# Performance work log

Measured on AMD Instinct MI355X. Metric: run time of the kernel, lower is better.

Reference implementation:

```python
import jax, jax.numpy as jnp
import numpy as np

D_MODEL = 512
NUM_HEADS = 8
VOCAB = 32000
B, TQ, TS = 4, 512, 512


def setup_inputs() -> dict:
    key = jax.random.key(0)
    ks = jax.random.split(key, 12)
    s = 1.0 / np.sqrt(D_MODEL)
    inp = {
        "src_vocab_size": VOCAB,
        "dec_output": jax.random.normal(ks[0], (B, TQ, D_MODEL), jnp.float32),
        "enc_output": jax.random.normal(ks[1], (B, TS, D_MODEL), jnp.float32),
        "src": jax.random.randint(ks[2], (B, TS), 0, VOCAB),
        "p1": jax.random.uniform(ks[3], (B, TQ, VOCAB), jnp.float32),
        # fcQ: d_model -> d_model (xavier)
        "WfcQ": jax.random.normal(ks[4], (D_MODEL, D_MODEL), jnp.float32) * s,
        "bfcQ": jnp.zeros((D_MODEL,), jnp.float32),
        # MHA query / key projections (V and output proj skipped in copy mode)
        "Wq": jax.random.normal(ks[5], (D_MODEL, D_MODEL), jnp.float32) * s,
        "bq": jnp.zeros((D_MODEL,), jnp.float32),
        "Wk": jax.random.normal(ks[6], (D_MODEL, D_MODEL), jnp.float32) * s,
        "bk": jnp.zeros((D_MODEL,), jnp.float32),
        # fcw: d_model -> 1 gate
        "Wfcw": jax.random.normal(ks[7], (1, D_MODEL), jnp.float32) * s,
        "bfcw": jnp.zeros((1,), jnp.float32),
    }
    return inp


def reference(src_vocab_size, dec_output, enc_output, src, p1,
              WfcQ, bfcQ, Wq, bq, Wk, bk, Wfcw, bfcw):
    b, tq, d = dec_output.shape
    h = NUM_HEADS
    dh = d // h
    # copy_query = fcQ(dec_output)
    cq = dec_output @ WfcQ.T + bfcQ
    # per-head Q, K projections
    Q = (cq @ Wq.T + bq).reshape(b, tq, h, dh).transpose(0, 2, 1, 3)          # [b,h,tq,dh]
    K = (enc_output @ Wk.T + bk).reshape(b, -1, h, dh).transpose(0, 2, 1, 3)  # [b,h,ts,dh]
    scale = 1.0 / jnp.sqrt(jnp.asarray(dh, dec_output.dtype))
    scores = jnp.einsum('bhqd,bhkd->bhqk', Q, K) * scale
    attn = jax.nn.softmax(scores, axis=-1).mean(axis=1)  # [b,tq,ts] head-averaged
    # attn @ one_hot(src, vocab)  ==  scatter-add of attn weights by src token id
    def scatter_copy(a, s):  # a: [tq,ts], s: [ts]
        return jax.ops.segment_sum(a.T, s, num_segments=src_vocab_size).T  # [tq,vocab]
    a_output = jax.vmap(scatter_copy)(attn, src)  # [b,tq,vocab]
    p2 = jax.nn.softmax(a_output, axis=-1)
    w = jax.nn.sigmoid(dec_output @ Wfcw.T + bfcw)  # [b,tq,1]
    return p2 * w + (1.0 - w) * p1
```

## Files before the change

kernel.cpp:

```cpp
#include <hip/hip_runtime.h>

constexpr int BATCH = 4;
constexpr int SEQ   = 512;
constexpr int DM    = 512;
constexpr int NH    = 8;
constexpr int HD    = 64;
constexpr int NV    = 32000;
constexpr int NROWS = BATCH * SEQ;

__device__ __forceinline__ float wave_reduce_max(float v) {
#pragma unroll
  for (int o = 32; o > 0; o >>= 1) v = fmaxf(v, __shfl_down(v, o, 64));
  return v;
}
__device__ __forceinline__ float wave_reduce_sum(float v) {
#pragma unroll
  for (int o = 32; o > 0; o >>= 1) v += __shfl_down(v, o, 64);
  return v;
}

__global__ __launch_bounds__(256)
void gemm_bias_kernel(const float* __restrict__ A, const float* __restrict__ W,
                      const float* __restrict__ bias, float* __restrict__ C,
                      int M, int N, int K) {
  __shared__ float As[16][68];
  __shared__ float Ws[16][68];
  const int tid = threadIdx.x;
  const int tx = tid & 15, ty = tid >> 4;
  const int m0 = blockIdx.y << 6, n0 = blockIdx.x << 6;
  const int r = tid >> 2;
  const int c = (tid & 3) << 2;
  float acc[4][4] = {};
  for (int k0 = 0; k0 < K; k0 += 16) {
    float4 av = *(const float4*)(A + (size_t)(m0 + r) * K + k0 + c);
    float4 wv = *(const float4*)(W + (size_t)(n0 + r) * K + k0 + c);
    As[c + 0][r] = av.x; As[c + 1][r] = av.y; As[c + 2][r] = av.z; As[c + 3][r] = av.w;
    Ws[c + 0][r] = wv.x; Ws[c + 1][r] = wv.y; Ws[c + 2][r] = wv.z; Ws[c + 3][r] = wv.w;
    __syncthreads();
#pragma unroll
    for (int kk = 0; kk < 16; ++kk) {
      float4 a4 = *(const float4*)(&As[kk][ty << 2]);
      float4 b4 = *(const float4*)(&Ws[kk][tx << 2]);
      float a[4] = {a4.x, a4.y, a4.z, a4.w};
      float b[4] = {b4.x, b4.y, b4.z, b4.w};
#pragma unroll
      for (int i = 0; i < 4; ++i)
#pragma unroll
        for (int j = 0; j < 4; ++j) acc[i][j] = fmaf(a[i], b[j], acc[i][j]);
    }
    __syncthreads();
  }
#pragma unroll
  for (int i = 0; i < 4; ++i) {
    const int m = m0 + (ty << 2) + i;
#pragma unroll
    for (int j = 0; j < 4; ++j) {
      const int n = n0 + (tx << 2) + j;
      C[(size_t)m * N + n] = acc[i][j] + bias[n];
    }
  }
}

__global__ __launch_bounds__(256)
void scores_kernel(const float* __restrict__ Qlin, const float* __restrict__ Klin,
                   float* __restrict__ scores) {
  const int bh = blockIdx.z, bb = bh >> 3, h = bh & 7;
  const int tq0 = blockIdx.y << 6, ts0 = blockIdx.x << 6;
  __shared__ float Qs[64 * 65];
  __shared__ float Ks[64 * 65];
  const int tid = threadIdx.x;
#pragma unroll
  for (int i = 0; i < 4; ++i) {
    const int idx = tid + (i << 8);
    const int rr = idx >> 4, cc = (idx & 15) << 2;
    float4 qv = *(const float4*)(Qlin + (size_t)(bb * SEQ + tq0 + rr) * DM + h * HD + cc);
    Qs[rr * 65 + cc + 0] = qv.x; Qs[rr * 65 + cc + 1] = qv.y;
    Qs[rr * 65 + cc + 2] = qv.z; Qs[rr * 65 + cc + 3] = qv.w;
    float4 kv = *(const float4*)(Klin + (size_t)(bb * SEQ + ts0 + rr) * DM + h * HD + cc);
    Ks[rr * 65 + cc + 0] = kv.x; Ks[rr * 65 + cc + 1] = kv.y;
    Ks[rr * 65 + cc + 2] = kv.z; Ks[rr * 65 + cc + 3] = kv.w;
  }
  __syncthreads();
  const int tx = tid & 15, ty = tid >> 4;
  float acc[4][4] = {};
#pragma unroll 4
  for (int k = 0; k < 64; ++k) {
    float a[4], b[4];
#pragma unroll
    for (int i = 0; i < 4; ++i) a[i] = Qs[(ty * 4 + i) * 65 + k];
#pragma unroll
    for (int j = 0; j < 4; ++j) b[j] = Ks[(tx * 4 + j) * 65 + k];
#pragma unroll
    for (int i = 0; i < 4; ++i)
#pragma unroll
      for (int j = 0; j < 4; ++j) acc[i][j] = fmaf(a[i], b[j], acc[i][j]);
  }
#pragma unroll
  for (int i = 0; i < 4; ++i) {
    const int tq = tq0 + ty * 4 + i;
#pragma unroll
    for (int j = 0; j < 4; ++j) {
      const int ts = ts0 + tx * 4 + j;
      scores[((size_t)bh * SEQ + tq) * SEQ + ts] = acc[i][j] * 0.125f;
    }
  }
}

__global__ __launch_bounds__(256)
void softmax_mean_kernel(const float* __restrict__ scores, float* __restrict__ attn) {
  __shared__ float redm[4], reds[4];
  const int row = blockIdx.x;
  const int bb = row >> 9, tq = row & 511;
  const int tid = threadIdx.x;
  const int wid = tid >> 6, lane = tid & 63;
  float acc0 = 0.f, acc1 = 0.f;
  for (int h = 0; h < NH; ++h) {
    const float* srow = scores + ((size_t)(bb * NH + h) * SEQ + tq) * SEQ;
    const float s0 = srow[tid], s1 = srow[tid + 256];
    float m = wave_reduce_max(fmaxf(s0, s1));
    __syncthreads();
    if (lane == 0) redm[wid] = m;
    __syncthreads();
    m = fmaxf(fmaxf(redm[0], redm[1]), fmaxf(redm[2], redm[3]));
    const float e0 = __expf(s0 - m), e1 = __expf(s1 - m);
    float s = wave_reduce_sum(e0 + e1);
    __syncthreads();
    if (lane == 0) reds[wid] = s;
    __syncthreads();
    s = reds[0] + reds[1] + reds[2] + reds[3];
    const float inv = 1.f / s;
    acc0 = fmaf(e0, inv, acc0);
    acc1 = fmaf(e1, inv, acc1);
  }
  attn[(size_t)row * SEQ + tid]       = acc0 * 0.125f;
  attn[(size_t)row * SEQ + tid + 256] = acc1 * 0.125f;
}

__global__ void build_map_kernel(const int* __restrict__ src, int* __restrict__ map) {
  const int bb = blockIdx.x, ts = threadIdx.x;
  const int v = src[bb * SEQ + ts];
  atomicCAS(&map[(size_t)bb * NV + v], -1, ts);
}

__global__ void scatter_kernel(const float* __restrict__ attn, const int* __restrict__ src,
                               const int* __restrict__ map, float* __restrict__ aslots) {
  const int row = blockIdx.x, bb = row >> 9, ts = threadIdx.x;
  const int v = src[bb * SEQ + ts];
  const int rep = map[(size_t)bb * NV + v];
  atomicAdd(&aslots[(size_t)row * SEQ + rep], attn[(size_t)row * SEQ + ts]);
}

__global__ __launch_bounds__(256)
void row_stats_kernel(float* __restrict__ aslots, const float* __restrict__ dec,
                      const float* __restrict__ Wfcw, const float* __restrict__ bfcw,
                      float* __restrict__ row_a, float* __restrict__ row_b) {
  __shared__ float red1[4], red2[4];
  const int row = blockIdx.x, tid = threadIdx.x;
  const int wid = tid >> 6, lane = tid & 63;
  const float a0 = aslots[(size_t)row * SEQ + tid];
  const float a1 = aslots[(size_t)row * SEQ + tid + 256];
  const float e0 = __expf(a0), e1 = __expf(a1);
  aslots[(size_t)row * SEQ + tid] = e0;
  aslots[(size_t)row * SEQ + tid + 256] = e1;
  const float es = wave_reduce_sum(e0 + e1);
  const float d = dec[(size_t)row * DM + tid] * Wfcw[tid] +
                  dec[(size_t)row * DM + tid + 256] * Wfcw[tid + 256];
  const float ds = wave_reduce_sum(d);
  if (lane == 0) { red1[wid] = es; red2[wid] = ds; }
  __syncthreads();
  if (tid == 0) {
    const float esum = red1[0] + red1[1] + red1[2] + red1[3];
    const float dsum = red2[0] + red2[1] + red2[2] + red2[3] + bfcw[0];
    const float w = 1.f / (1.f + __expf(-dsum));
    const float denom = (float)(NV - SEQ) + esum;
    row_a[row] = 1.f - w;
    row_b[row] = w / denom;
  }
}

__global__ __launch_bounds__(256)
void final_kernel(const float* __restrict__ p1, const int* __restrict__ map,
                  const float* __restrict__ expa, const float* __restrict__ row_a,
                  const float* __restrict__ row_b, float* __restrict__ out) {
  const size_t g = (size_t)blockIdx.x * 256 + threadIdx.x;
  const int row = (int)(g / (NV / 4));
  const int q4  = (int)(g % (NV / 4));
  const int bb = row >> 9;
  const float4 p = ((const float4*)p1)[g];
  const int4 m = *(const int4*)(map + (size_t)bb * NV + (q4 << 2));
  const float ra = row_a[row], rb = row_b[row];
  const float* ea = expa + (size_t)row * SEQ;
  const float e0 = (m.x >= 0) ? ea[m.x] : 1.f;
  const float e1 = (m.y >= 0) ? ea[m.y] : 1.f;
  const float e2 = (m.z >= 0) ? ea[m.z] : 1.f;
  const float e3 = (m.w >= 0) ? ea[m.w] : 1.f;
  float4 o;
  o.x = fmaf(ra, p.x, rb * e0);
  o.y = fmaf(ra, p.y, rb * e1);
  o.z = fmaf(ra, p.z, rb * e2);
  o.w = fmaf(ra, p.w, rb * e3);
  ((float4*)out)[g] = o;
}

extern "C" void kernel_launch(void* const* d_in, const int* in_sizes, int n_in,
                              void* d_out, int out_size, void* d_ws, size_t ws_size,
                              hipStream_t stream) {
  const float* dec  = (const float*)d_in[1];
  const float* enc  = (const float*)d_in[2];
  const int*   src  = (const int*)d_in[3];
  const float* p1   = (const float*)d_in[4];
  const float* WfcQ = (const float*)d_in[5];
  const float* bfcQ = (const float*)d_in[6];
  const float* Wq   = (const float*)d_in[7];
  const float* bq   = (const float*)d_in[8];
  const float* Wk   = (const float*)d_in[9];
  const float* bk   = (const float*)d_in[10];
  const float* Wfcw = (const float*)d_in[11];
  const float* bfcw = (const float*)d_in[12];
  float* out = (float*)d_out;

  char* ws = (char*)d_ws;
  float* qlin   = (float*)(ws);
  float* klin   = (float*)(ws + (size_t)(4  << 20));
  float* attn   = (float*)(ws + (size_t)(8  << 20));
  float* aslots = (float*)(ws + (size_t)(12 << 20));
  int*   map    = (int*)  (ws + (size_t)(16 << 20));
  float* row_a  = (float*)(ws + (size_t)(17 << 20));
  float* row_b  = (float*)(ws + (size_t)(17 << 20) + 16384);
  float* scores = (float*)(ws + (size_t)(18 << 20));
  float* cq     = scores;

  hipMemsetAsync(map, 0xFF, (size_t)BATCH * NV * sizeof(int), stream);
  hipMemsetAsync(aslots, 0, (size_t)NROWS * SEQ * sizeof(float), stream);

  build_map_kernel<<<BATCH, SEQ, 0, stream>>>(src, map);

  dim3 gg(DM / 64, NROWS / 64);
  gemm_bias_kernel<<<gg, 256, 0, stream>>>(dec, WfcQ, bfcQ, cq,   NROWS, DM, DM);
  gemm_bias_kernel<<<gg, 256, 0, stream>>>(cq,  Wq,   bq,   qlin, NROWS, DM, DM);
  gemm_bias_kernel<<<gg, 256, 0, stream>>>(enc, Wk,   bk,   klin, NROWS, DM, DM);

  dim3 sg(SEQ / 64, SEQ / 64, BATCH * NH);
  scores_kernel<<<sg, 256, 0, stream>>>(qlin, klin, scores);

  softmax_mean_kernel<<<NROWS, 256, 0, stream>>>(scores, attn);
  scatter_kernel<<<NROWS, SEQ, 0, stream>>>(attn, src, map, aslots);
  row_stats_kernel<<<NROWS, 256, 0, stream>>>(aslots, dec, Wfcw, bfcw, row_a, row_b);

  final_kernel<<<(NROWS * (NV / 4)) / 256, 256, 0, stream>>>(p1, map, aslots, row_a, row_b, out);
}
```

Measured before the change: 588.2 us.

## Use bf16 MFMA GEMMs, fold fcQ into Wq, fuse softmax-scatter-stats

Inputs and K weights are converted to bf16, and the two Q-side linear layers are folded into one weight matrix and bias, so Q and K are computed by a single bf16 MFMA GEMM launch. The score computation also uses MFMA and writes bf16 scores. Head-softmax, head averaging, scatter into slots, exponentiation and the gate statistics are fused into one block-per-row kernel that uses shared-memory atomics. This removes fp32 FMA GEMMs, several intermediate buffers and launches, and the aslots memset, at the cost of bf16 rounding in the projections and scores.

```diff
diff --git a/kernel.cpp b/kernel.cpp
--- a/kernel.cpp
+++ b/kernel.cpp
@@ -4,10 +4,12 @@
 constexpr int SEQ   = 512;
 constexpr int DM    = 512;
 constexpr int NH    = 8;
-constexpr int HD    = 64;
 constexpr int NV    = 32000;
 constexpr int NROWS = BATCH * SEQ;
 
+typedef short short8 __attribute__((ext_vector_type(8)));
+typedef float floatx4 __attribute__((ext_vector_type(4)));
+
 __device__ __forceinline__ float wave_reduce_max(float v) {
 #pragma unroll
   for (int o = 32; o > 0; o >>= 1) v = fmaxf(v, __shfl_down(v, o, 64));
@@ -18,122 +20,162 @@
   for (int o = 32; o > 0; o >>= 1) v += __shfl_down(v, o, 64);
   return v;
 }
-
-__global__ __launch_bounds__(256)
-void gemm_bias_kernel(const float* __restrict__ A, const float* __restrict__ W,
-                      const float* __restrict__ bias, float* __restrict__ C,
-                      int M, int N, int K) {
+__device__ __forceinline__ unsigned short f2bf(float f) {
+  unsigned u = __float_as_uint(f);
+  u += 0x7FFFu + ((u >> 16) & 1u);
+  return (unsigned short)(u >> 16);
+}
+__device__ __forceinline__ float bf2f(unsigned short b) {
+  return __uint_as_float(((unsigned)b) << 16);
+}
+
+__global__ __launch_bounds__(256)
+void convert_bf16_kernel(const float* __restrict__ in, unsigned short* __restrict__ out, int n4) {
+  const int i = blockIdx.x * 256 + threadIdx.x;
+  if (i < n4) {
+    const float4 v = ((const float4*)in)[i];
+    ushort4 o;
+    o.x = f2bf(v.x); o.y = f2bf(v.y); o.z = f2bf(v.z); o.w = f2bf(v.w);
+    ((ushort4*)out)[i] = o;
+  }
+}
+
+__global__ __launch_bounds__(256)
+void wfold_kernel(const float* __restrict__ Wq, const float* __restrict__ WfcQ,
+                  unsigned short* __restrict__ Wqc) {
   __shared__ float As[16][68];
-  __shared__ float Ws[16][68];
+  __shared__ float Bs[16][68];
+  const int tid = threadIdx.x, tx = tid & 15, ty = tid >> 4;
+  const int m0 = blockIdx.y << 6, n0 = blockIdx.x << 6;
+  const int r = tid >> 2, c = (tid & 3) << 2;
+  float acc[4][4] = {};
+  for (int k0 = 0; k0 < DM; k0 += 16) {
+    const float4 av = *(const float4*)(Wq + (size_t)(m0 + r) * DM + k0 + c);
+    As[c + 0][r] = av.x; As[c + 1][r] = av.y; As[c + 2][r] = av.z; As[c + 3][r] = av.w;
+    const float4 bv = *(const float4*)(WfcQ + (size_t)(k0 + ty) * DM + n0 + (tx << 2));
+    *(float4*)(&Bs[ty][tx << 2]) = bv;
+    __syncthreads();
+#pragma unroll
+    for (int kk = 0; kk < 16; ++kk) {
+      const float4 a4 = *(const float4*)(&As[kk][ty << 2]);
+      const float4 b4 = *(const float4*)(&Bs[kk][tx << 2]);
+      const float a[4] = {a4.x, a4.y, a4.z, a4.w};
+      const float b[4] = {b4.x, b4.y, b4.z, b4.w};
+#pragma unroll
+      for (int i = 0; i < 4; ++i)
+#pragma unroll
+        for (int j = 0; j < 4; ++j) acc[i][j] = fmaf(a[i], b[j], acc[i][j]);
+    }
+    __syncthreads();
+  }
+#pragma unroll
+  for (int i = 0; i < 4; ++i)
+#pragma unroll
+    for (int j = 0; j < 4; ++j)
+      Wqc[(size_t)(m0 + (ty << 2) + i) * DM + n0 + (tx << 2) + j] = f2bf(acc[i][j]);
+}
+
+__global__ __launch_bounds__(512)
+void bias_fold_kernel(const float* __restrict__ Wq, const float* __restrict__ bfcQ,
+                      const float* __restrict__ bq, float* __restrict__ bq2) {
+  const int tid = threadIdx.x, h = tid >> 6, l = tid & 63;
+  const int n = blockIdx.x * 8 + h;
+  float s = 0.f;
+#pragma unroll
+  for (int t = 0; t < 8; ++t) {
+    const int j = l + 64 * t;
+    s = fmaf(Wq[(size_t)n * DM + j], bfcQ[j], s);
+  }
+  s = wave_reduce_sum(s);
+  if (l == 0) bq2[n] = bq[n] + s;
+}
+
+__global__ __launch_bounds__(256)
+void gemm_mfma_kernel(const unsigned short* __restrict__ A0, const unsigned short* __restrict__ W0,
+                      const float* __restrict__ b0, unsigned short* __restrict__ C0,
+                      const unsigned short* __restrict__ A1, const unsigned short* __restrict__ W1,
+                      const float* __restrict__ b1, unsigned short* __restrict__ C1) {
+  const unsigned short* A; const unsigned short* W; const float* bias; unsigned short* C;
+  if (blockIdx.z == 0) { A = A0; W = W0; bias = b0; C = C0; }
+  else                 { A = A1; W = W1; bias = b1; C = C1; }
+  const int m0 = blockIdx.y << 6, n0 = blockIdx.x << 6;
+  __shared__ __align__(16) unsigned short As[64 * 72];
+  __shared__ __align__(16) unsigned short Ws[64 * 72];
   const int tid = threadIdx.x;
-  const int tx = tid & 15, ty = tid >> 4;
-  const int m0 = blockIdx.y << 6, n0 = blockIdx.x << 6;
-  const int r = tid >> 2;
-  const int c = (tid & 3) << 2;
-  float acc[4][4] = {};
-  for (int k0 = 0; k0 < K; k0 += 16) {
-    float4 av = *(const float4*)(A + (size_t)(m0 + r) * K + k0 + c);
-    float4 wv = *(const float4*)(W + (size_t)(n0 + r) * K + k0 + c);
-    As[c + 0][r] = av.x; As[c + 1][r] = av.y; As[c + 2][r] = av.z; As[c + 3][r] = av.w;
-    Ws[c + 0][r] = wv.x; Ws[c + 1][r] = wv.y; Ws[c + 2][r] = wv.z; Ws[c + 3][r] = wv.w;
+  const int wv = tid >> 6, l = tid & 63;
+  const int lm = l & 15, lq = l >> 4;
+  floatx4 acc[4] = {};
+  for (int k0 = 0; k0 < DM; k0 += 64) {
+#pragma unroll
+    for (int i = 0; i < 2; ++i) {
+      const int ch = tid + (i << 8);
+      const int row = ch >> 3, c8 = (ch & 7) << 3;
+      *(int4*)(&As[row * 72 + c8]) = *(const int4*)(A + (size_t)(m0 + row) * DM + k0 + c8);
+      *(int4*)(&Ws[row * 72 + c8]) = *(const int4*)(W + (size_t)(n0 + row) * DM + k0 + c8);
+    }
     __syncthreads();
 #pragma unroll
-    for (int kk = 0; kk < 16; ++kk) {
-      float4 a4 = *(const float4*)(&As[kk][ty << 2]);
-      float4 b4 = *(const float4*)(&Ws[kk][tx << 2]);
-      float a[4] = {a4.x, a4.y, a4.z, a4.w};
-      float b[4] = {b4.x, b4.y, b4.z, b4.w};
-#pragma unroll
-      for (int i = 0; i < 4; ++i)
-#pragma unroll
-        for (int j = 0; j < 4; ++j) acc[i][j] = fmaf(a[i], b[j], acc[i][j]);
+    for (int ks = 0; ks < 64; ks += 32) {
+      const short8 a = *(const short8*)(&As[(16 * wv + lm) * 72 + ks + lq * 8]);
+#pragma unroll
+      for (int c = 0; c < 4; ++c) {
+        const short8 b = *(const short8*)(&Ws[(16 * c + lm) * 72 + ks + lq * 8]);
+        acc[c] = __builtin_amdgcn_mfma_f32_16x16x32_bf16(a, b, acc[c], 0, 0, 0);
+      }
     }
     __syncthreads();
   }
 #pragma unroll
-  for (int i = 0; i < 4; ++i) {
-    const int m = m0 + (ty << 2) + i;
-#pragma unroll
-    for (int j = 0; j < 4; ++j) {
-      const int n = n0 + (tx << 2) + j;
-      C[(size_t)m * N + n] = acc[i][j] + bias[n];
-    }
-  }
-}
-
-__global__ __launch_bounds__(256)
-void scores_kernel(const float* __restrict__ Qlin, const float* __restrict__ Klin,
-                   float* __restrict__ scores) {
+  for (int c = 0; c < 4; ++c) {
+    const int col = n0 + 16 * c + lm;
+    const float bv = bias[col];
+#pragma unroll
+    for (int r = 0; r < 4; ++r) {
+      const int row = m0 + 16 * wv + lq * 4 + r;
+      C[(size_t)row * DM + col] = f2bf(acc[c][r] + bv);
+    }
+  }
+}
+
+__global__ __launch_bounds__(256)
+void scores_mfma_kernel(const unsigned short* __restrict__ Q, const unsigned short* __restrict__ Kk,
+                        unsigned short* __restrict__ scores) {
   const int bh = blockIdx.z, bb = bh >> 3, h = bh & 7;
   const int tq0 = blockIdx.y << 6, ts0 = blockIdx.x << 6;
-  __shared__ float Qs[64 * 65];
-  __shared__ float Ks[64 * 65];
+  __shared__ __align__(16) unsigned short Qs[64 * 72];
+  __shared__ __align__(16) unsigned short Ks[64 * 72];
   const int tid = threadIdx.x;
-#pragma unroll
-  for (int i = 0; i < 4; ++i) {
-    const int idx = tid + (i << 8);
-    const int rr = idx >> 4, cc = (idx & 15) << 2;
-    float4 qv = *(const float4*)(Qlin + (size_t)(bb * SEQ + tq0 + rr) * DM + h * HD + cc);
-    Qs[rr * 65 + cc + 0] = qv.x; Qs[rr * 65 + cc + 1] = qv.y;
-    Qs[rr * 65 + cc + 2] = qv.z; Qs[rr * 65 + cc + 3] = qv.w;
-    float4 kv = *(const float4*)(Klin + (size_t)(bb * SEQ + ts0 + rr) * DM + h * HD + cc);
-    Ks[rr * 65 + cc + 0] = kv.x; Ks[rr * 65 + cc + 1] = kv.y;
-    Ks[rr * 65 + cc + 2] = kv.z; Ks[rr * 65 + cc + 3] = kv.w;
+  const int wv = tid >> 6, l = tid & 63;
+  const int lm = l & 15, lq = l >> 4;
+#pragma unroll
+  for (int i = 0; i < 2; ++i) {
+    const int ch = tid + (i << 8);
+    const int row = ch >> 3, c8 = (ch & 7) << 3;
+    *(int4*)(&Qs[row * 72 + c8]) =
+        *(const int4*)(Q + (size_t)(bb * SEQ + tq0 + row) * DM + h * 64 + c8);
+    *(int4*)(&Ks[row * 72 + c8]) =
+        *(const int4*)(Kk + (size_t)(bb * SEQ + ts0 + row) * DM + h * 64 + c8);
   }
   __syncthreads();
-  const int tx = tid & 15, ty = tid >> 4;
-  float acc[4][4] = {};
-#pragma unroll 4
-  for (int k = 0; k < 64; ++k) {
-    float a[4], b[4];
-#pragma unroll
-    for (int i = 0; i < 4; ++i) a[i] = Qs[(ty * 4 + i) * 65 + k];
-#pragma unroll
-    for (int j = 0; j < 4; ++j) b[j] = Ks[(tx * 4 + j) * 65 + k];
-#pragma unroll
-    for (int i = 0; i < 4; ++i)
-#pragma unroll
-      for (int j = 0; j < 4; ++j) acc[i][j] = fmaf(a[i], b[j], acc[i][j]);
-  }
-#pragma unroll
-  for (int i = 0; i < 4; ++i) {
-    const int tq = tq0 + ty * 4 + i;
-#pragma unroll
-    for (int j = 0; j < 4; ++j) {
-      const int ts = ts0 + tx * 4 + j;
-      scores[((size_t)bh * SEQ + tq) * SEQ + ts] = acc[i][j] * 0.125f;
-    }
-  }
-}
-
-__global__ __launch_bounds__(256)
-void softmax_mean_kernel(const float* __restrict__ scores, float* __restrict__ attn) {
-  __shared__ float redm[4], reds[4];
-  const int row = blockIdx.x;
-  const int bb = row >> 9, tq = row & 511;
-  const int tid = threadIdx.x;
-  const int wid = tid >> 6, lane = tid & 63;
-  float acc0 = 0.f, acc1 = 0.f;
-  for (int h = 0; h < NH; ++h) {
-    const float* srow = scores + ((size_t)(bb * NH + h) * SEQ + tq) * SEQ;
-    const float s0 = srow[tid], s1 = srow[tid + 256];
-    float m = wave_reduce_max(fmaxf(s0, s1));
-    __syncthreads();
-    if (lane == 0) redm[wid] = m;
-    __syncthreads();
-    m = fmaxf(fmaxf(redm[0], redm[1]), fmaxf(redm[2], redm[3]));
-    const float e0 = __expf(s0 - m), e1 = __expf(s1 - m);
-    float s = wave_reduce_sum(e0 + e1);
-    __syncthreads();
-    if (lane == 0) reds[wid] = s;
-    __syncthreads();
-    s = reds[0] + reds[1] + reds[2] + reds[3];
-    const float inv = 1.f / s;
-    acc0 = fmaf(e0, inv, acc0);
-    acc1 = fmaf(e1, inv, acc1);
-  }
-  attn[(size_t)row * SEQ + tid]       = acc0 * 0.125f;
-  attn[(size_t)row * SEQ + tid + 256] = acc1 * 0.125f;
+  floatx4 acc[4] = {};
+#pragma unroll
+  for (int ks = 0; ks < 64; ks += 32) {
+    const short8 a = *(const short8*)(&Qs[(16 * wv + lm) * 72 + ks + lq * 8]);
+#pragma unroll
+    for (int c = 0; c < 4; ++c) {
+      const short8 b = *(const short8*)(&Ks[(16 * c + lm) * 72 + ks + lq * 8]);
+      acc[c] = __builtin_amdgcn_mfma_f32_16x16x32_bf16(a, b, acc[c], 0, 0, 0);
+    }
+  }
+#pragma unroll
+  for (int c = 0; c < 4; ++c) {
+    const int ts = ts0 + 16 * c + lm;
+#pragma unroll
+    for (int r = 0; r < 4; ++r) {
+      const int tq = tq0 + 16 * wv + lq * 4 + r;
+      scores[((size_t)bh * SEQ + tq) * SEQ + ts] = f2bf(acc[c][r] * 0.125f);
+    }
+  }
 }
 
 __global__ void build_map_kernel(const int* __restrict__ src, int* __restrict__ map) {
@@ -142,39 +184,63 @@
   atomicCAS(&map[(size_t)bb * NV + v], -1, ts);
 }
 
-__global__ void scatter_kernel(const float* __restrict__ attn, const int* __restrict__ src,
-                               const int* __restrict__ map, float* __restrict__ aslots) {
-  const int row = blockIdx.x, bb = row >> 9, ts = threadIdx.x;
-  const int v = src[bb * SEQ + ts];
-  const int rep = map[(size_t)bb * NV + v];
-  atomicAdd(&aslots[(size_t)row * SEQ + rep], attn[(size_t)row * SEQ + ts]);
-}
-
-__global__ __launch_bounds__(256)
-void row_stats_kernel(float* __restrict__ aslots, const float* __restrict__ dec,
-                      const float* __restrict__ Wfcw, const float* __restrict__ bfcw,
-                      float* __restrict__ row_a, float* __restrict__ row_b) {
-  __shared__ float red1[4], red2[4];
-  const int row = blockIdx.x, tid = threadIdx.x;
-  const int wid = tid >> 6, lane = tid & 63;
-  const float a0 = aslots[(size_t)row * SEQ + tid];
-  const float a1 = aslots[(size_t)row * SEQ + tid + 256];
-  const float e0 = __expf(a0), e1 = __expf(a1);
-  aslots[(size_t)row * SEQ + tid] = e0;
-  aslots[(size_t)row * SEQ + tid + 256] = e1;
-  const float es = wave_reduce_sum(e0 + e1);
-  const float d = dec[(size_t)row * DM + tid] * Wfcw[tid] +
-                  dec[(size_t)row * DM + tid + 256] * Wfcw[tid + 256];
-  const float ds = wave_reduce_sum(d);
-  if (lane == 0) { red1[wid] = es; red2[wid] = ds; }
+__global__ __launch_bounds__(512)
+void softmax_fused_kernel(const unsigned short* __restrict__ scores, const int* __restrict__ src,
+                          const int* __restrict__ map, const float* __restrict__ dec,
+                          const float* __restrict__ Wfcw, const float* __restrict__ bfcw,
+                          float* __restrict__ expa, float* __restrict__ row_a,
+                          float* __restrict__ row_b) {
+  __shared__ float hp[8 * 520];
+  __shared__ float aslot[512];
+  __shared__ float r1[8], r2[8];
+  const int row = blockIdx.x, bb = row >> 9, tq = row & 511;
+  const int tid = threadIdx.x, h = tid >> 6, l = tid & 63;
+  aslot[tid] = 0.f;
+  const unsigned short* srow = scores + ((size_t)(bb * NH + h) * SEQ + tq) * SEQ;
+  union { int4 v; unsigned short u[8]; } U;
+  U.v = *(const int4*)(srow + 8 * l);
+  float s[8];
+#pragma unroll
+  for (int i = 0; i < 8; ++i) s[i] = bf2f(U.u[i]);
+  float m = s[0];
+#pragma unroll
+  for (int i = 1; i < 8; ++i) m = fmaxf(m, s[i]);
+  m = wave_reduce_max(m);
+  m = __shfl(m, 0, 64);
+  float e[8], sum = 0.f;
+#pragma unroll
+  for (int i = 0; i < 8; ++i) { e[i] = __expf(s[i] - m); sum += e[i]; }
+  sum = wave_reduce_sum(sum);
+  sum = __shfl(sum, 0, 64);
+  const float inv = 1.f / sum;
+  float4 p0, p1v;
+  p0.x = e[0] * inv; p0.y = e[1] * inv; p0.z = e[2] * inv; p0.w = e[3] * inv;
+  p1v.x = e[4] * inv; p1v.y = e[5] * inv; p1v.z = e[6] * inv; p1v.w = e[7] * inv;
+  *(float4*)(&hp[h * 520 + 8 * l])     = p0;
+  *(float4*)(&hp[h * 520 + 8 * l + 4]) = p1v;
+  __syncthreads();
+  float a = 0.f;
+#pragma unroll
+  for (int h2 = 0; h2 < 8; ++h2) a += hp[h2 * 520 + tid];
+  a *= 0.125f;
+  const int sv = src[bb * SEQ + tid];
+  const int rep = map[(size_t)bb * NV + sv];
+  atomicAdd(&aslot[rep], a);
+  __syncthreads();
+  const float ev = __expf(aslot[tid]);
+  expa[(size_t)row * SEQ + tid] = ev;
+  const float d = dec[(size_t)row * DM + tid] * Wfcw[tid];
+  float es = wave_reduce_sum(ev);
+  float ds = wave_reduce_sum(d);
+  if (l == 0) { r1[h] = es; r2[h] = ds; }
   __syncthreads();
   if (tid == 0) {
-    const float esum = red1[0] + red1[1] + red1[2] + red1[3];
-    const float dsum = red2[0] + red2[1] + red2[2] + red2[3] + bfcw[0];
+    float esum = 0.f, dsum = bfcw[0];
+#pragma unroll
+    for (int i = 0; i < 8; ++i) { esum += r1[i]; dsum += r2[i]; }
     const float w = 1.f / (1.f + __expf(-dsum));
-    const float denom = (float)(NV - SEQ) + esum;
     row_a[row] = 1.f - w;
-    row_b[row] = w / denom;
+    row_b[row] = w / ((float)(NV - SEQ) + esum);
   }
 }
 
@@ -220,32 +286,36 @@
   float* out = (float*)d_out;
 
   char* ws = (char*)d_ws;
-  float* qlin   = (float*)(ws);
-  float* klin   = (float*)(ws + (size_t)(4  << 20));
-  float* attn   = (float*)(ws + (size_t)(8  << 20));
-  float* aslots = (float*)(ws + (size_t)(12 << 20));
-  int*   map    = (int*)  (ws + (size_t)(16 << 20));
-  float* row_a  = (float*)(ws + (size_t)(17 << 20));
-  float* row_b  = (float*)(ws + (size_t)(17 << 20) + 16384);
-  float* scores = (float*)(ws + (size_t)(18 << 20));
-  float* cq     = scores;
+  int*            map     = (int*)(ws);
+  unsigned short* dec_bf  = (unsigned short*)(ws + (size_t)( 1 << 20));
+  unsigned short* enc_bf  = (unsigned short*)(ws + (size_t)( 3 << 20));
+  unsigned short* wk_bf   = (unsigned short*)(ws + (size_t)( 5 << 20));
+  unsigned short* wqc_bf  = (unsigned short*)(ws + (size_t)( 5 << 20) + (512 << 10));
+  float*          bq2     = (float*)(ws + (size_t)( 6 << 20));
+  float*          row_a   = (float*)(ws + (size_t)( 6 << 20) + (64 << 10));
+  float*          row_b   = (float*)(ws + (size_t)( 6 << 20) + (128 << 10));
+  unsigned short* qlin_bf = (unsigned short*)(ws + (size_t)( 7 << 20));
+  unsigned short* klin_bf = (unsigned short*)(ws + (size_t)( 9 << 20));
+  float*          expa    = (float*)(ws + (size_t)(11 << 20));
+  unsigned short* scores  = (unsigned short*)(ws + (size_t)(16 << 20));
 
   hipMemsetAsync(map, 0xFF, (size_t)BATCH * NV * sizeof(int), stream);
-  hipMemsetAsync(aslots, 0, (size_t)NROWS * SEQ * sizeof(float), stream);
-
   build_map_kernel<<<BATCH, SEQ, 0, stream>>>(src, map);
 
-  dim3 gg(DM / 64, NROWS / 64);
-  gemm_bias_kernel<<<gg, 256, 0, stream>>>(dec, WfcQ, bfcQ, cq,   NROWS, DM, DM);
-  gemm_bias_kernel<<<gg, 256, 0, stream>>>(cq,  Wq,   bq,   qlin, NROWS, DM, DM);
-  gemm_bias_kernel<<<gg, 256, 0, stream>>>(enc, Wk,   bk,   klin, NROWS, DM, DM);
-
-  dim3 sg(SEQ / 64, SEQ / 64, BATCH * NH);
-  scores_kernel<<<sg, 256, 0, stream>>>(qlin, klin, scores);
-
-  softmax_mean_kernel<<<NROWS, 256, 0, stream>>>(scores, attn);
-  scatter_kernel<<<NROWS, SEQ, 0, stream>>>(attn, src, map, aslots);
-  row_stats_kernel<<<NROWS, 256, 0, stream>>>(aslots, dec, Wfcw, bfcw, row_a, row_b);
-
-  final_kernel<<<(NROWS * (NV / 4)) / 256, 256, 0, stream>>>(p1, map, aslots, row_a, row_b, out);
-}
+  convert_bf16_kernel<<<1024, 256, 0, stream>>>(dec, dec_bf, NROWS * DM / 4);
+  convert_bf16_kernel<<<1024, 256, 0, stream>>>(enc, enc_bf, NROWS * DM / 4);
+  convert_bf16_kernel<<<256, 256, 0, stream>>>(Wk, wk_bf, DM * DM / 4);
+
+  wfold_kernel<<<dim3(8, 8), 256, 0, stream>>>(Wq, WfcQ, wqc_bf);
+  bias_fold_kernel<<<64, 512, 0, stream>>>(Wq, bfcQ, bq, bq2);
+
+  gemm_mfma_kernel<<<dim3(8, 32, 2), 256, 0, stream>>>(
+      dec_bf, wqc_bf, bq2, qlin_bf, enc_bf, wk_bf, bk, klin_bf);
+
+  scores_mfma_kernel<<<dim3(8, 8, 32), 256, 0, stream>>>(qlin_bf, klin_bf, scores);
+
+  softmax_fused_kernel<<<NROWS, 512, 0, stream>>>(scores, src, map, dec, Wfcw, bfcw,
+                                                  expa, row_a, row_b);
+
+  final_kernel<<<(NROWS * (NV / 4)) / 256, 256, 0, stream>>>(p1, map, expa, row_a, row_b, out);
+}
```

After: 518.9 us. 1.13x faster.
